# Kernel tuning notes

Measured on AMD Instinct MI355X. Metric: run time of the kernel, lower is better.

Reference implementation:

```python
import jax, jax.numpy as jnp
import numpy as np

V, E, H, L = 32000, 256, 512, 2
B, S, T = 32, 128, 128

def _run_lstm(xs, layers, h0, c0):
    # xs: [B,T,in]; layers: list of (Wih[4H,in], Whh[4H,H], bih[4H], bhh[4H]); h0,c0: [L,B,H]
    def step(carry, x):
        h, c = carry
        inp = x
        hs, cs = [], []
        for l, (Wih, Whh, bih, bhh) in enumerate(layers):
            g = inp @ Wih.T + h[l] @ Whh.T + bih + bhh
            i, f, gg, o = jnp.split(g, 4, axis=-1)  # torch gate order: i, f, g, o
            cn = jax.nn.sigmoid(f) * c[l] + jax.nn.sigmoid(i) * jnp.tanh(gg)
            hn = jax.nn.sigmoid(o) * jnp.tanh(cn)
            hs.append(hn); cs.append(cn); inp = hn
        return (jnp.stack(hs), jnp.stack(cs)), inp
    (hT, cT), ys = jax.lax.scan(step, (h0, c0), jnp.swapaxes(xs, 0, 1))
    return jnp.swapaxes(ys, 0, 1), hT, cT

def setup_inputs():
    key = jax.random.key(0)
    ks = jax.random.split(key, 24)
    k = 1.0 / np.sqrt(H)
    u = lambda kk, shape: jax.random.uniform(kk, shape, jnp.float32, -k, k)
    inp = {
        "src": jax.random.randint(ks[0], (B, S), 0, V),
        "tgt": jax.random.randint(ks[1], (B, T), 0, V),
        "emb": jax.random.normal(ks[2], (V, E), jnp.float32) * 0.02,
        "Wout": u(ks[3], (V, H)),
        "bout": u(ks[4], (V,)),
    }
    i = 5
    for pre in ("enc", "dec"):
        for l in range(L):
            din = E if l == 0 else H
            inp[pre + "_Wih" + str(l)] = u(ks[i], (4 * H, din)); i += 1
            inp[pre + "_Whh" + str(l)] = u(ks[i], (4 * H, H)); i += 1
            inp[pre + "_bih" + str(l)] = u(ks[i], (4 * H,)); i += 1
            inp[pre + "_bhh" + str(l)] = u(ks[i], (4 * H,)); i += 1
    return inp

def reference(src, tgt, emb, Wout, bout,
              enc_Wih0, enc_Whh0, enc_bih0, enc_bhh0,
              enc_Wih1, enc_Whh1, enc_bih1, enc_bhh1,
              dec_Wih0, dec_Whh0, dec_bih0, dec_bhh0,
              dec_Wih1, dec_Whh1, dec_bih1, dec_bhh1):
    enc_layers = [(enc_Wih0, enc_Whh0, enc_bih0, enc_bhh0),
                  (enc_Wih1, enc_Whh1, enc_bih1, enc_bhh1)]
    dec_layers = [(dec_Wih0, dec_Whh0, dec_bih0, dec_bhh0),
                  (dec_Wih1, dec_Whh1, dec_bih1, dec_bhh1)]
    h0 = jnp.zeros((L, src.shape[0], H), jnp.float32)
    c0 = jnp.zeros_like(h0)
    src_embed = emb[src]                                   # [B,S,E]; dropout = identity (eval)
    _, hT, cT = _run_lstm(src_embed, enc_layers, h0, c0)
    tgt_embed = emb[tgt]                                   # full teacher forcing (ratio=1.0)
    dec_out, _, _ = _run_lstm(tgt_embed, dec_layers, hT, cT)  # [B,T,H]
    logits = jnp.einsum('bth,vh->btv', dec_out, Wout) + bout  # [B,T,V]
    return logits
```

## Files before the change

### kernel.cpp

```cpp
#include <hip/hip_runtime.h>
#include <math.h>

#define Bsz 32
#define Hd  512
#define SEQ 128
#define G4H 2048
#define BH  16384
#define BARSTRIDE 32
#define SLOT 16384

typedef __attribute__((ext_vector_type(8))) short bf16x8;
typedef __attribute__((ext_vector_type(4))) float f32x4;
typedef __attribute__((ext_vector_type(4))) unsigned short us4;

__device__ __forceinline__ void gload16(const void* g, void* l) {
  __builtin_amdgcn_global_load_lds(
      (const __attribute__((address_space(1))) unsigned int*)g,
      (__attribute__((address_space(3))) unsigned int*)l, 16, 0, 0);
}

__global__ __launch_bounds__(256) void bias_sum_k(const float* __restrict__ a,
                                                  const float* __restrict__ b,
                                                  float* __restrict__ out) {
  int i = blockIdx.x * 256 + threadIdx.x;
  if (i < G4H) out[i] = a[i] + b[i];
}

__global__ __launch_bounds__(256) void embed_k(const int* __restrict__ idx,
                                               const float* __restrict__ emb,
                                               float* __restrict__ out) {
  int t = blockIdx.x * 256 + threadIdx.x;
  int m = t >> 6, e4 = (t & 63) << 2;
  *(float4*)&out[(size_t)m * 256 + e4] =
      *(const float4*)&emb[(size_t)idx[m] * 256 + e4];
}

__global__ __launch_bounds__(256) void split_k(const float* __restrict__ X,
                                               unsigned short* __restrict__ hi,
                                               unsigned short* __restrict__ lo) {
  int i = (blockIdx.x * 256 + threadIdx.x) << 2;
  float4 x = *(const float4*)&X[i];
  const float* xp = (const float*)&x;
  us4 h, l;
  #pragma unroll
  for (int e = 0; e < 4; ++e) {
    float v = xp[e];
    unsigned int u = __float_as_uint(v);
    unsigned int hr = (u + 0x7fffu + ((u >> 16) & 1u)) & 0xffff0000u;
    h[e] = (unsigned short)(hr >> 16);
    float rem = v - __uint_as_float(hr);
    unsigned int u2 = __float_as_uint(rem);
    l[e] = (unsigned short)((u2 + 0x7fffu + ((u2 >> 16) & 1u)) >> 16);
  }
  *(us4*)&hi[i] = h;
  *(us4*)&lo[i] = l;
}

__global__ __launch_bounds__(256) void pack_wbf_k(const float* __restrict__ W,
                                                  unsigned short* __restrict__ out) {
  __shared__ float Wl[16][512];
// ... 66 lines not shown
    for (int mf = 0; mf < 4; ++mf) {
      afh[mf] = *(const bf16x8*)&Ash[(wr * 64 + mf * 16 + fr) * 32 + fk];
      afl[mf] = *(const bf16x8*)&Asl[(wr * 64 + mf * 16 + fr) * 32 + fk];
    }
    #pragma unroll
    for (int nf = 0; nf < 4; ++nf) {
      bfh[nf] = *(const bf16x8*)&Bsh[(wc * 64 + nf * 16 + fr) * 32 + fk];
      bfl[nf] = *(const bf16x8*)&Bsl[(wc * 64 + nf * 16 + fr) * 32 + fk];
    }
    #pragma unroll
    for (int mf = 0; mf < 4; ++mf)
      #pragma unroll
      for (int nf = 0; nf < 4; ++nf) {
        acc[mf][nf] = __builtin_amdgcn_mfma_f32_16x16x32_bf16(afh[mf], bfh[nf],
                                                              acc[mf][nf], 0, 0, 0);
        acc[mf][nf] = __builtin_amdgcn_mfma_f32_16x16x32_bf16(afh[mf], bfl[nf],
                                                              acc[mf][nf], 0, 0, 0);
        acc[mf][nf] = __builtin_amdgcn_mfma_f32_16x16x32_bf16(afl[mf], bfh[nf],
                                                              acc[mf][nf], 0, 0, 0);
      }
    __syncthreads();
  }

  const int rgrp = (lane >> 4) << 2;
  #pragma unroll
  for (int nf = 0; nf < 4; ++nf) {
    int n = n0 + wc * 64 + nf * 16 + fr;
    float bn = bias[n];
    #pragma unroll
    for (int mf = 0; mf < 4; ++mf) {
      #pragma unroll
      for (int r = 0; r < 4; ++r) {
        int m = m0 + wr * 64 + mf * 16 + rgrp + r;
        C[(size_t)m * ldc + n] = acc[mf][nf][r] + bn;
      }
    }
  }
}

__device__ __forceinline__ void pollwait(const int* arr, int target) {
  const int tid = threadIdx.x;
  if (tid < 64) {
    const int* p0 = &arr[tid * BARSTRIDE];
    const int* p1 = &arr[(tid + 64) * BARSTRIDE];
    for (;;) {
      int a = __hip_atomic_load(p0, __ATOMIC_RELAXED, __HIP_MEMORY_SCOPE_AGENT);
      int b = __hip_atomic_load(p1, __ATOMIC_RELAXED, __HIP_MEMORY_SCOPE_AGENT);
      if (__all(min(a, b) >= target)) break;
      __builtin_amdgcn_s_sleep(1);
    }
  }
  __syncthreads();
}

__global__ __launch_bounds__(256, 1)
void lstm_seq_k(const unsigned short* __restrict__ pw0,
                const unsigned short* __restrict__ pw1a,
                const unsigned short* __restrict__ pw1b,
                const float* __restrict__ x0pre,
                const float* __restrict__ bias1,
                unsigned short* __restrict__ h0hi, unsigned short* __restrict__ h0lo,
                unsigned short* __restrict__ h1hi, unsigned short* __restrict__ h1lo,
                const unsigned short* __restrict__ h0ihi, const unsigned short* __restrict__ h0ilo,
                const unsigned short* __restrict__ h1ihi, const unsigned short* __restrict__ h1ilo,
                const float* __restrict__ c0init, const float* __restrict__ c1init,
                float* __restrict__ c0fin, float* __restrict__ c1fin,
                int* __restrict__ flag)
{
  __shared__ unsigned short wlds[49152];
  __shared__ float gpart[6528];
  __shared__ float gx[512];
  __shared__ unsigned short hstage[512];

  const int blk = blockIdx.x, tid = threadIdx.x;
  const int w = tid >> 6, lane = tid & 63;
  const int fr = lane & 15, fgk = (lane >> 4) << 3;

  {
    const uint4* s0 = (const uint4*)(pw0 + (size_t)blk * 16384);
    const uint4* s1 = (const uint4*)(pw1a + (size_t)blk * 16384);
    const uint4* s2 = (const uint4*)(pw1b + (size_t)blk * 16384);
    uint4* d = (uint4*)wlds;
    for (int i = tid; i < 2048; i += 256) {
      d[i] = s0[i]; d[2048 + i] = s1[i]; d[4096 + i] = s2[i];
    }
  }

  const int cl = (tid >> 5) & 3, b2 = tid & 31;
  const int nn = blk * 4 + cl;
  float creg, bv0 = 0.f, bv1 = 0.f, bv2 = 0.f, bv3 = 0.f;
  if (tid < 128) {
    creg = c0init[b2 * 512 + nn];
  } else {
    creg = c1init[b2 * 512 + nn];
    bv0 = bias1[nn]; bv1 = bias1[512 + nn];
    bv2 = bias1[1024 + nn]; bv3 = bias1[1536 + nn];
  }
  const int xcol = tid & 15, xb = tid >> 4;
  const int xj = (xcol >> 2) * 512 + blk * 4 + (xcol & 3);
  __syncthreads();

  #pragma unroll 1
  for (int u = 0; u <= SEQ; ++u) {
    const bool doL0 = (u < SEQ), doL1 = (u >= 1);

    float xv0 = 0.f, xv1 = 0.f;
    if (doL0) {
      xv0 = x0pre[((size_t)xb * SEQ + u) * G4H + xj];
      xv1 = x0pre[((size_t)(xb + 16) * SEQ + u) * G4H + xj];
    }

    if (u > 0) pollwait(flag, u);

    if (doL0) { gx[xcol * 32 + xb] = xv0; gx[xcol * 32 + xb + 16] = xv1; }

    const unsigned short* hAh = (u == 0) ? h0ihi : h0hi + (size_t)(u - 1) * SLOT;
    const unsigned short* hAl = (u == 0) ? h0ilo : h0lo + (size_t)(u - 1) * SLOT;
    const unsigned short* hBh = (u <= 1) ? h1ihi : h1hi + (size_t)(u - 2) * SLOT;
    const unsigned short* hBl = (u <= 1) ? h1ilo : h1lo + (size_t)(u - 2) * SLOT;

    f32x4 acc[3][2];
    #pragma unroll
    for (int m = 0; m < 3; ++m) {
      acc[m][0] = (f32x4){0.f, 0.f, 0.f, 0.f};
      acc[m][1] = (f32x4){0.f, 0.f, 0.f, 0.f};
    }

    #pragma unroll
    for (int q = 0; q < 4; ++q) {
      const int kf = (w << 2) + q;
      const int ko = (kf << 5) + fgk;
      const int wko = (kf << 9) + lane * 8;
      bf16x8 ah0 = *(const bf16x8*)&hAh[(size_t)fr * 512 + ko];
      bf16x8 al0 = *(const bf16x8*)&hAl[(size_t)fr * 512 + ko];
      bf16x8 ah1 = *(const bf16x8*)&hAh[(size_t)(fr + 16) * 512 + ko];
      bf16x8 al1 = *(const bf16x8*)&hAl[(size_t)(fr + 16) * 512 + ko];
      if (doL0) {
        bf16x8 bh = *(const bf16x8*)&wlds[wko];
        bf16x8 bl = *(const bf16x8*)&wlds[8192 + wko];
        acc[0][0] = __builtin_amdgcn_mfma_f32_16x16x32_bf16(ah0, bh, acc[0][0], 0, 0, 0);
        acc[0][0] = __builtin_amdgcn_mfma_f32_16x16x32_bf16(ah0, bl, acc[0][0], 0, 0, 0);
        acc[0][0] = __builtin_amdgcn_mfma_f32_16x16x32_bf16(al0, bh, acc[0][0], 0, 0, 0);
        acc[0][1] = __builtin_amdgcn_mfma_f32_16x16x32_bf16(ah1, bh, acc[0][1], 0, 0, 0);
        acc[0][1] = __builtin_amdgcn_mfma_f32_16x16x32_bf16(ah1, bl, acc[0][1], 0, 0, 0);
        acc[0][1] = __builtin_amdgcn_mfma_f32_16x16x32_bf16(al1, bh, acc[0][1], 0, 0, 0);
      }
      if (doL1) {
        bf16x8 bh = *(const bf16x8*)&wlds[16384 + wko];
        bf16x8 bl = *(const bf16x8*)&wlds[16384 + 8192 + wko];
        acc[1][0] = __builtin_amdgcn_mfma_f32_16x16x32_bf16(ah0, bh, acc[1][0], 0, 0, 0);
        acc[1][0] = __builtin_amdgcn_mfma_f32_16x16x32_bf16(ah0, bl, acc[1][0], 0, 0, 0);
        acc[1][0] = __builtin_amdgcn_mfma_f32_16x16x32_bf16(al0, bh, acc[1][0], 0, 0, 0);
        acc[1][1] = __builtin_amdgcn_mfma_f32_16x16x32_bf16(ah1, bh, acc[1][1], 0, 0, 0);
        acc[1][1] = __builtin_amdgcn_mfma_f32_16x16x32_bf16(ah1, bl, acc[1][1], 0, 0, 0);
        acc[1][1] = __builtin_amdgcn_mfma_f32_16x16x32_bf16(al1, bh, acc[1][1], 0, 0, 0);
        bf16x8 ch0 = *(const bf16x8*)&hBh[(size_t)fr * 512 + ko];
        bf16x8 cl0 = *(const bf16x8*)&hBl[(size_t)fr * 512 + ko];
        bf16x8 ch1 = *(const bf16x8*)&hBh[(size_t)(fr + 16) * 512 + ko];
        bf16x8 cl1 = *(const bf16x8*)&hBl[(size_t)(fr + 16) * 512 + ko];
        bf16x8 dh = *(const bf16x8*)&wlds[32768 + wko];
        bf16x8 dl = *(const bf16x8*)&wlds[32768 + 8192 + wko];
        acc[2][0] = __builtin_amdgcn_mfma_f32_16x16x32_bf16(ch0, dh, acc[2][0], 0, 0, 0);
        acc[2][0] = __builtin_amdgcn_mfma_f32_16x16x32_bf16(ch0, dl, acc[2][0], 0, 0, 0);
        acc[2][0] = __builtin_amdgcn_mfma_f32_16x16x32_bf16(cl0, dh, acc[2][0], 0, 0, 0);
        acc[2][1] = __builtin_amdgcn_mfma_f32_16x16x32_bf16(ch1, dh, acc[2][1], 0, 0, 0);
        acc[2][1] = __builtin_amdgcn_mfma_f32_16x16x32_bf16(ch1, dl, acc[2][1], 0, 0, 0);
        acc[2][1] = __builtin_amdgcn_mfma_f32_16x16x32_bf16(cl1, dh, acc[2][1], 0, 0, 0);
      }
    }

    #pragma unroll
    for (int m = 0; m < 3; ++m)
      #pragma unroll
      for (int mf = 0; mf < 2; ++mf)
        #pragma unroll
        for (int j = 0; j < 4; ++j)
          gpart[(m * 4 + w) * 544 + (mf * 16 + (lane >> 4) * 4 + j) * 17 + fr] = acc[m][mf][j];
    __syncthreads();

    if (tid < 128) {
      if (doL0) {
        float g[4];
        #pragma unroll
        for (int gt = 0; gt < 4; ++gt) {
          float s = gx[(gt * 4 + cl) * 32 + b2];
          #pragma unroll
          for (int ww = 0; ww < 4; ++ww)
            s += gpart[ww * 544 + b2 * 17 + gt * 4 + cl];
          g[gt] = s;
        }
        float i_ = 1.f / (1.f + expf(-g[0]));
        float f_ = 1.f / (1.f + expf(-g[1]));
        float gg = tanhf(g[2]);
        float o_ = 1.f / (1.f + expf(-g[3]));
        float cn = f_ * creg + i_ * gg;
        float hn = o_ * tanhf(cn);
        creg = cn;
        unsigned int uu = __float_as_uint(hn);
        unsigned int hr = (uu + 0x7fffu + ((uu >> 16) & 1u)) & 0xffff0000u;
        float rem = hn - __uint_as_float(hr);
        unsigned int u2 = __float_as_uint(rem);
        hstage[(0 * 32 + b2) * 4 + cl] = (unsigned short)(hr >> 16);
        hstage[(1 * 32 + b2) * 4 + cl] =
            (unsigned short)((u2 + 0x7fffu + ((u2 >> 16) & 1u)) >> 16);
      }
    } else {
      if (doL1) {
        float g[4];
        #pragma unroll
        for (int gt = 0; gt < 4; ++gt) {
          float s = 0.f;
          #pragma unroll
          for (int ww = 0; ww < 4; ++ww)
            s += gpart[(4 + ww) * 544 + b2 * 17 + gt * 4 + cl]
               + gpart[(8 + ww) * 544 + b2 * 17 + gt * 4 + cl];
          g[gt] = s;
        }
        g[0] += bv0; g[1] += bv1; g[2] += bv2; g[3] += bv3;
        float i_ = 1.f / (1.f + expf(-g[0]));
        float f_ = 1.f / (1.f + expf(-g[1]));
        float gg = tanhf(g[2]);
        float o_ = 1.f / (1.f + expf(-g[3]));
        float cn = f_ * creg + i_ * gg;
        float hn = o_ * tanhf(cn);
        creg = cn;
        unsigned int uu = __float_as_uint(hn);
        unsigned int hr = (uu + 0x7fffu + ((uu >> 16) & 1u)) & 0xffff0000u;
        float rem = hn - __uint_as_float(hr);
        unsigned int u2 = __float_as_uint(rem);
        hstage[(2 * 32 + b2) * 4 + cl] = (unsigned short)(hr >> 16);
        hstage[(3 * 32 + b2) * 4 + cl] =
            (unsigned short)((u2 + 0x7fffu + ((u2 >> 16) & 1u)) >> 16);
      }
    }
    __syncthreads();

    if (tid < 128) {
      int layer = tid >> 6, hl = (tid >> 5) & 1, bb = tid & 31;
      bool go = layer ? doL1 : doL0;
      if (go) {
        unsigned long long v =
            *(const unsigned long long*)&hstage[((layer * 2 + hl) * 32 + bb) * 4];
        unsigned short* arr = layer ? (hl ? h1lo : h1hi) : (hl ? h0lo : h0hi);
        int slot = layer ? (u - 1) : u;
        __hip_atomic_store((unsigned long long*)&arr[(size_t)slot * SLOT + bb * 512 + blk * 4],
                           v, __ATOMIC_RELAXED, __HIP_MEMORY_SCOPE_AGENT);
      }
    }
    asm volatile("s_waitcnt vmcnt(0)" ::: "memory");
    __syncthreads();
    if (tid == 0)
      __hip_atomic_store(&flag[blk * BARSTRIDE], u + 1,
                         __ATOMIC_RELAXED, __HIP_MEMORY_SCOPE_AGENT);
  }

  if (tid < 128) c0fin[b2 * 512 + nn] = creg;
  else           c1fin[b2 * 512 + nn] = creg;
}

extern "C" void kernel_launch(void* const* d_in, const int* in_sizes, int n_in,
                              void* d_out, int out_size, void* d_ws, size_t ws_size,
                              hipStream_t stream) {
  const int*   src  = (const int*)d_in[0];
  const int*   tgt  = (const int*)d_in[1];
  const float* emb  = (const float*)d_in[2];
  const float* Wout = (const float*)d_in[3];
  const float* bout = (const float*)d_in[4];
  const float* eWih0 = (const float*)d_in[5];
  const float* eWhh0 = (const float*)d_in[6];
  const float* ebih0 = (const float*)d_in[7];
  const float* ebhh0 = (const float*)d_in[8];
  const float* eWih1 = (const float*)d_in[9];
  const float* eWhh1 = (const float*)d_in[10];
  const float* ebih1 = (const float*)d_in[11];
  const float* ebhh1 = (const float*)d_in[12];
  const float* dWih0 = (const float*)d_in[13];
  const float* dWhh0 = (const float*)d_in[14];
  const float* dbih0 = (const float*)d_in[15];
  const float* dbhh0 = (const float*)d_in[16];
  const float* dWih1 = (const float*)d_in[17];
  const float* dWhh1 = (const float*)d_in[18];
  const float* dbih1 = (const float*)d_in[19];
  const float* dbhh1 = (const float*)d_in[20];

  if (ws_size < 86245376ull) return;

  float* ws = (float*)d_ws;
  char*  wsb = (char*)d_ws;
  unsigned short* PK   = (unsigned short*)(wsb + 37748736);
  unsigned short* PW0E = PK;
  unsigned short* PW1AE = PK + 2097152;
  unsigned short* PW1BE = PK + 4194304;
  unsigned short* PW0D = PK + 6291456;
  unsigned short* PW1AD = PK + 8388608;
  unsigned short* PW1BD = PK + 10485760;
  const size_t OFF_EMB  = 0;
  const size_t OFF_X0   = 1048576;
  const size_t OFF_BS0E = 15728640;
  const size_t OFF_B1E  = 15730688;
  const size_t OFF_BS0D = 15732736;
  const size_t OFF_B1D  = 15734784;
  const size_t OFF_Z    = 15736832;
  const size_t OFF_BAR  = 15753216;
  const size_t OFF_C0   = 15761408;
  const size_t OFF_C1   = 15777792;
  unsigned short* Ehi  = (unsigned short*)(wsb + 63176704);
  unsigned short* Elo  = (unsigned short*)(wsb + 65273856);
  unsigned short* WIhi = (unsigned short*)(wsb + 67371008);
  unsigned short* WIlo = (unsigned short*)(wsb + 68419584);
  unsigned short* H0hi = (unsigned short*)(wsb + 69468160);
  unsigned short* H0lo = (unsigned short*)(wsb + 73662464);
  unsigned short* H1hi = (unsigned short*)(wsb + 77856768);
  unsigned short* H1lo = (unsigned short*)(wsb + 82051072);
  unsigned short* Bhi  = (unsigned short*)(wsb + 0);
  unsigned short* Blo  = (unsigned short*)(wsb + 32768000);
  const unsigned short* ZU = (const unsigned short*)(ws + OFF_Z);
  const float* ZF = ws + OFF_Z;

  int* eflag = (int*)(ws + OFF_BAR);
  int* dflag = eflag + 4096;

  pack_wbf_k<<<128, 256, 0, stream>>>(eWhh0, PW0E);
  pack_wbf_k<<<128, 256, 0, stream>>>(eWih1, PW1AE);
  pack_wbf_k<<<128, 256, 0, stream>>>(eWhh1, PW1BE);
  pack_wbf_k<<<128, 256, 0, stream>>>(dWhh0, PW0D);
  pack_wbf_k<<<128, 256, 0, stream>>>(dWih1, PW1AD);
  pack_wbf_k<<<128, 256, 0, stream>>>(dWhh1, PW1BD);
  bias_sum_k<<<8, 256, 0, stream>>>(ebih0, ebhh0, ws + OFF_BS0E);
  bias_sum_k<<<8, 256, 0, stream>>>(ebih1, ebhh1, ws + OFF_B1E);
  bias_sum_k<<<8, 256, 0, stream>>>(dbih0, dbhh0, ws + OFF_BS0D);
  bias_sum_k<<<8, 256, 0, stream>>>(dbih1, dbhh1, ws + OFF_B1D);

  hipMemsetAsync(ws + OFF_Z, 0, 98304, stream);

  embed_k<<<1024, 256, 0, stream>>>(src, emb, ws + OFF_EMB);
  split_k<<<1024, 256, 0, stream>>>(ws + OFF_EMB, Ehi, Elo);
  split_k<<<512, 256, 0, stream>>>(eWih0, WIhi, WIlo);
  gemm_bfs_k<<<dim3(32, 16), 256, 0, stream>>>(Ehi, Elo, WIhi, WIlo,
                                               ws + OFF_BS0E, ws + OFF_X0, 256, 2048, 0);
  lstm_seq_k<<<128, 256, 0, stream>>>(PW0E, PW1AE, PW1BE,
                                      ws + OFF_X0, ws + OFF_B1E,
                                      H0hi, H0lo, H1hi, H1lo,
                                      ZU, ZU, ZU, ZU,
                                      ZF, ZF,
                                      ws + OFF_C0, ws + OFF_C1,
                                      eflag);

  embed_k<<<1024, 256, 0, stream>>>(tgt, emb, ws + OFF_EMB);
  split_k<<<1024, 256, 0, stream>>>(ws + OFF_EMB, Ehi, Elo);
  split_k<<<512, 256, 0, stream>>>(dWih0, WIhi, WIlo);
  gemm_bfs_k<<<dim3(32, 16), 256, 0, stream>>>(Ehi, Elo, WIhi, WIlo,
                                               ws + OFF_BS0D, ws + OFF_X0, 256, 2048, 0);
  lstm_seq_k<<<128, 256, 0, stream>>>(PW0D, PW1AD, PW1BD,
                                      ws + OFF_X0, ws + OFF_B1D,
                                      H0hi, H0lo, H1hi, H1lo,
                                      H0hi + (size_t)127 * SLOT, H0lo + (size_t)127 * SLOT,
                                      H1hi + (size_t)127 * SLOT, H1lo + (size_t)127 * SLOT,
                                      ws + OFF_C0, ws + OFF_C1,
                                      ws + OFF_C0, ws + OFF_C1,
                                      dflag);

  split_k<<<16000, 256, 0, stream>>>(Wout, Bhi, Blo);
  gemm_bfs_k<<<dim3(32, 250), 256, 0, stream>>>(H1hi, H1lo, Bhi, Blo,
                                                bout, (float*)d_out, 512, 32000, 1);
}
```

Before: 2.220 ms.

## Split LSTM layer phases with separate flags to overlap layer-1 and layer-0 steps

Restructures the persistent two-layer LSTM loop so each iteration first does layer 1 for step u-2, publishes a layer-1 flag, then does layer 0 for step u with its own flag barrier. Layer 0 no longer waits for layer-1 completion in the same barrier. This shortens the critical path of the layer-0 recurrence, which now only depends on the previous layer-0 step. In exchange it adds a second grid-wide poll per iteration, an extra loop iteration, and relocated flag and cell-state buffers in the workspace.

```diff
diff --git a/kernel.cpp b/kernel.cpp
--- a/kernel.cpp
+++ b/kernel.cpp
@@ -178,6 +178,21 @@
   }
   __syncthreads();
 }
+__device__ __forceinline__ void pollwait2(const int* a1, int t1,
+                                          const int* a0, int t0) {
+  const int tid = threadIdx.x;
+  if (tid < 64) {
+    for (;;) {
+      int a = __hip_atomic_load(&a1[tid * BARSTRIDE], __ATOMIC_RELAXED, __HIP_MEMORY_SCOPE_AGENT);
+      int b = __hip_atomic_load(&a1[(tid + 64) * BARSTRIDE], __ATOMIC_RELAXED, __HIP_MEMORY_SCOPE_AGENT);
+      int c = __hip_atomic_load(&a0[tid * BARSTRIDE], __ATOMIC_RELAXED, __HIP_MEMORY_SCOPE_AGENT);
+      int d = __hip_atomic_load(&a0[(tid + 64) * BARSTRIDE], __ATOMIC_RELAXED, __HIP_MEMORY_SCOPE_AGENT);
+      if (__all(min(a, b) >= t1 && min(c, d) >= t0)) break;
+      __builtin_amdgcn_s_sleep(1);
+    }
+  }
+  __syncthreads();
+}
 
 __global__ __launch_bounds__(256, 1)
 void lstm_seq_k(const unsigned short* __restrict__ pw0,
@@ -191,7 +206,7 @@
                 const unsigned short* __restrict__ h1ihi, const unsigned short* __restrict__ h1ilo,
                 const float* __restrict__ c0init, const float* __restrict__ c1init,
                 float* __restrict__ c0fin, float* __restrict__ c1fin,
-                int* __restrict__ flag)
+                int* __restrict__ flag0, int* __restrict__ flag1)
 {
   __shared__ unsigned short wlds[49152];
   __shared__ float gpart[6528];
@@ -227,8 +242,9 @@
   __syncthreads();
 
   #pragma unroll 1
-  for (int u = 0; u <= SEQ; ++u) {
-    const bool doL0 = (u < SEQ), doL1 = (u >= 1);
+  for (int u = 0; u <= SEQ + 1; ++u) {
+    const bool doL0 = (u < SEQ), doL1 = (u >= 2);
+    const int t1 = u - 2;
 
     float xv0 = 0.f, xv1 = 0.f;
     if (doL0) {
@@ -236,102 +252,61 @@
       xv1 = x0pre[((size_t)(xb + 16) * SEQ + u) * G4H + xj];
     }
 
-    if (u > 0) pollwait(flag, u);
-
-    if (doL0) { gx[xcol * 32 + xb] = xv0; gx[xcol * 32 + xb + 16] = xv1; }
-
-    const unsigned short* hAh = (u == 0) ? h0ihi : h0hi + (size_t)(u - 1) * SLOT;
-    const unsigned short* hAl = (u == 0) ? h0ilo : h0lo + (size_t)(u - 1) * SLOT;
-    const unsigned short* hBh = (u <= 1) ? h1ihi : h1hi + (size_t)(u - 2) * SLOT;
-    const unsigned short* hBl = (u <= 1) ? h1ilo : h1lo + (size_t)(u - 2) * SLOT;
-
-    f32x4 acc[3][2];
-    #pragma unroll
-    for (int m = 0; m < 3; ++m) {
-      acc[m][0] = (f32x4){0.f, 0.f, 0.f, 0.f};
-      acc[m][1] = (f32x4){0.f, 0.f, 0.f, 0.f};
-    }
-
-    #pragma unroll
-    for (int q = 0; q < 4; ++q) {
-      const int kf = (w << 2) + q;
-      const int ko = (kf << 5) + fgk;
-      const int wko = (kf << 9) + lane * 8;
-      bf16x8 ah0 = *(const bf16x8*)&hAh[(size_t)fr * 512 + ko];
-      bf16x8 al0 = *(const bf16x8*)&hAl[(size_t)fr * 512 + ko];
-      bf16x8 ah1 = *(const bf16x8*)&hAh[(size_t)(fr + 16) * 512 + ko];
-      bf16x8 al1 = *(const bf16x8*)&hAl[(size_t)(fr + 16) * 512 + ko];
-      if (doL0) {
-        bf16x8 bh = *(const bf16x8*)&wlds[wko];
-        bf16x8 bl = *(const bf16x8*)&wlds[8192 + wko];
+    if (u >= 1) pollwait2(flag1, u - 1, flag0, u - 1);
+
+    if (doL1) {
+      const unsigned short* hAh = h0hi + (size_t)t1 * SLOT;
+      const unsigned short* hAl = h0lo + (size_t)t1 * SLOT;
+      const unsigned short* hBh = (t1 == 0) ? h1ihi : h1hi + (size_t)(t1 - 1) * SLOT;
+      const unsigned short* hBl = (t1 == 0) ? h1ilo : h1lo + (size_t)(t1 - 1) * SLOT;
+
+      f32x4 acc[2][2];
+      #pragma unroll
+      for (int m = 0; m < 2; ++m) {
+        acc[m][0] = (f32x4){0.f, 0.f, 0.f, 0.f};
+        acc[m][1] = (f32x4){0.f, 0.f, 0.f, 0.f};
+      }
+      #pragma unroll
+      for (int q = 0; q < 4; ++q) {
+        const int kf = (w << 2) + q;
+        const int ko = (kf << 5) + fgk;
+        const int wko = (kf << 9) + lane * 8;
+        bf16x8 ah0 = *(const bf16x8*)&hAh[(size_t)fr * 512 + ko];
+        bf16x8 al0 = *(const bf16x8*)&hAl[(size_t)fr * 512 + ko];
+        bf16x8 ah1 = *(const bf16x8*)&hAh[(size_t)(fr + 16) * 512 + ko];
+        bf16x8 al1 = *(const bf16x8*)&hAl[(size_t)(fr + 16) * 512 + ko];
+        bf16x8 bh = *(const bf16x8*)&wlds[16384 + wko];
+        bf16x8 bl = *(const bf16x8*)&wlds[16384 + 8192 + wko];
         acc[0][0] = __builtin_amdgcn_mfma_f32_16x16x32_bf16(ah0, bh, acc[0][0], 0, 0, 0);
         acc[0][0] = __builtin_amdgcn_mfma_f32_16x16x32_bf16(ah0, bl, acc[0][0], 0, 0, 0);
         acc[0][0] = __builtin_amdgcn_mfma_f32_16x16x32_bf16(al0, bh, acc[0][0], 0, 0, 0);
         acc[0][1] = __builtin_amdgcn_mfma_f32_16x16x32_bf16(ah1, bh, acc[0][1], 0, 0, 0);
         acc[0][1] = __builtin_amdgcn_mfma_f32_16x16x32_bf16(ah1, bl, acc[0][1], 0, 0, 0);
         acc[0][1] = __builtin_amdgcn_mfma_f32_16x16x32_bf16(al1, bh, acc[0][1], 0, 0, 0);
-      }
-      if (doL1) {
-        bf16x8 bh = *(const bf16x8*)&wlds[16384 + wko];
-        bf16x8 bl = *(const bf16x8*)&wlds[16384 + 8192 + wko];
-        acc[1][0] = __builtin_amdgcn_mfma_f32_16x16x32_bf16(ah0, bh, acc[1][0], 0, 0, 0);
-        acc[1][0] = __builtin_amdgcn_mfma_f32_16x16x32_bf16(ah0, bl, acc[1][0], 0, 0, 0);
-        acc[1][0] = __builtin_amdgcn_mfma_f32_16x16x32_bf16(al0, bh, acc[1][0], 0, 0, 0);
-        acc[1][1] = __builtin_amdgcn_mfma_f32_16x16x32_bf16(ah1, bh, acc[1][1], 0, 0, 0);
-        acc[1][1] = __builtin_amdgcn_mfma_f32_16x16x32_bf16(ah1, bl, acc[1][1], 0, 0, 0);
-        acc[1][1] = __builtin_amdgcn_mfma_f32_16x16x32_bf16(al1, bh, acc[1][1], 0, 0, 0);
         bf16x8 ch0 = *(const bf16x8*)&hBh[(size_t)fr * 512 + ko];
         bf16x8 cl0 = *(const bf16x8*)&hBl[(size_t)fr * 512 + ko];
         bf16x8 ch1 = *(const bf16x8*)&hBh[(size_t)(fr + 16) * 512 + ko];
         bf16x8 cl1 = *(const bf16x8*)&hBl[(size_t)(fr + 16) * 512 + ko];
         bf16x8 dh = *(const bf16x8*)&wlds[32768 + wko];
         bf16x8 dl = *(const bf16x8*)&wlds[32768 + 8192 + wko];
-        acc[2][0] = __builtin_amdgcn_mfma_f32_16x16x32_bf16(ch0, dh, acc[2][0], 0, 0, 0);
-        acc[2][0] = __builtin_amdgcn_mfma_f32_16x16x32_bf16(ch0, dl, acc[2][0], 0, 0, 0);
-        acc[2][0] = __builtin_amdgcn_mfma_f32_16x16x32_bf16(cl0, dh, acc[2][0], 0, 0, 0);
-        acc[2][1] = __builtin_amdgcn_mfma_f32_16x16x32_bf16(ch1, dh, acc[2][1], 0, 0, 0);
-        acc[2][1] = __builtin_amdgcn_mfma_f32_16x16x32_bf16(ch1, dl, acc[2][1], 0, 0, 0);
-        acc[2][1] = __builtin_amdgcn_mfma_f32_16x16x32_bf16(cl1, dh, acc[2][1], 0, 0, 0);
-      }
-    }
-
-    #pragma unroll
-    for (int m = 0; m < 3; ++m)
-      #pragma unroll
-      for (int mf = 0; mf < 2; ++mf)
+        acc[1][0] = __builtin_amdgcn_mfma_f32_16x16x32_bf16(ch0, dh, acc[1][0], 0, 0, 0);
+        acc[1][0] = __builtin_amdgcn_mfma_f32_16x16x32_bf16(ch0, dl, acc[1][0], 0, 0, 0);
+        acc[1][0] = __builtin_amdgcn_mfma_f32_16x16x32_bf16(cl0, dh, acc[1][0], 0, 0, 0);
+        acc[1][1] = __builtin_amdgcn_mfma_f32_16x16x32_bf16(ch1, dh, acc[1][1], 0, 0, 0);
+        acc[1][1] = __builtin_amdgcn_mfma_f32_16x16x32_bf16(ch1, dl, acc[1][1], 0, 0, 0);
+        acc[1][1] = __builtin_amdgcn_mfma_f32_16x16x32_bf16(cl1, dh, acc[1][1], 0, 0, 0);
+      }
+      #pragma unroll
+      for (int m = 0; m < 2; ++m)
         #pragma unroll
-        for (int j = 0; j < 4; ++j)
-          gpart[(m * 4 + w) * 544 + (mf * 16 + (lane >> 4) * 4 + j) * 17 + fr] = acc[m][mf][j];
-    __syncthreads();
-
-    if (tid < 128) {
-      if (doL0) {
-        float g[4];
-        #pragma unroll
-        for (int gt = 0; gt < 4; ++gt) {
-          float s = gx[(gt * 4 + cl) * 32 + b2];
+        for (int mf = 0; mf < 2; ++mf)
           #pragma unroll
-          for (int ww = 0; ww < 4; ++ww)
-            s += gpart[ww * 544 + b2 * 17 + gt * 4 + cl];
-          g[gt] = s;
-        }
-        float i_ = 1.f / (1.f + expf(-g[0]));
-        float f_ = 1.f / (1.f + expf(-g[1]));
-        float gg = tanhf(g[2]);
-        float o_ = 1.f / (1.f + expf(-g[3]));
-        float cn = f_ * creg + i_ * gg;
-        float hn = o_ * tanhf(cn);
-        creg = cn;
-        unsigned int uu = __float_as_uint(hn);
-        unsigned int hr = (uu + 0x7fffu + ((uu >> 16) & 1u)) & 0xffff0000u;
-        float rem = hn - __uint_as_float(hr);
-        unsigned int u2 = __float_as_uint(rem);
-        hstage[(0 * 32 + b2) * 4 + cl] = (unsigned short)(hr >> 16);
-        hstage[(1 * 32 + b2) * 4 + cl] =
-            (unsigned short)((u2 + 0x7fffu + ((u2 >> 16) & 1u)) >> 16);
-      }
-    } else {
-      if (doL1) {
+          for (int j = 0; j < 4; ++j)
+            gpart[((m + 1) * 4 + w) * 544 + (mf * 16 + (lane >> 4) * 4 + j) * 17 + fr]
+                = acc[m][mf][j];
+      __syncthreads();
+
+      if (tid >= 128) {
         float g[4];
         #pragma unroll
         for (int gt = 0; gt < 4; ++gt) {
@@ -358,26 +333,100 @@
         hstage[(3 * 32 + b2) * 4 + cl] =
             (unsigned short)((u2 + 0x7fffu + ((u2 >> 16) & 1u)) >> 16);
       }
-    }
-    __syncthreads();
-
-    if (tid < 128) {
-      int layer = tid >> 6, hl = (tid >> 5) & 1, bb = tid & 31;
-      bool go = layer ? doL1 : doL0;
-      if (go) {
+      __syncthreads();
+
+      if (tid >= 64 && tid < 128) {
+        int hl = (tid >> 5) & 1, bb = tid & 31;
         unsigned long long v =
-            *(const unsigned long long*)&hstage[((layer * 2 + hl) * 32 + bb) * 4];
-        unsigned short* arr = layer ? (hl ? h1lo : h1hi) : (hl ? h0lo : h0hi);
-        int slot = layer ? (u - 1) : u;
-        __hip_atomic_store((unsigned long long*)&arr[(size_t)slot * SLOT + bb * 512 + blk * 4],
+            *(const unsigned long long*)&hstage[((2 + hl) * 32 + bb) * 4];
+        unsigned short* arr = hl ? h1lo : h1hi;
+        __hip_atomic_store((unsigned long long*)&arr[(size_t)t1 * SLOT + bb * 512 + blk * 4],
                            v, __ATOMIC_RELAXED, __HIP_MEMORY_SCOPE_AGENT);
       }
-    }
-    asm volatile("s_waitcnt vmcnt(0)" ::: "memory");
-    __syncthreads();
+      asm volatile("s_waitcnt vmcnt(0)" ::: "memory");
+      __syncthreads();
+    }
     if (tid == 0)
-      __hip_atomic_store(&flag[blk * BARSTRIDE], u + 1,
+      __hip_atomic_store(&flag1[blk * BARSTRIDE], u,
                          __ATOMIC_RELAXED, __HIP_MEMORY_SCOPE_AGENT);
+
+    if (doL0) {
+      pollwait(flag0, u);
+
+      gx[xcol * 32 + xb] = xv0; gx[xcol * 32 + xb + 16] = xv1;
+
+      const unsigned short* hAh = (u == 0) ? h0ihi : h0hi + (size_t)(u - 1) * SLOT;
+      const unsigned short* hAl = (u == 0) ? h0ilo : h0lo + (size_t)(u - 1) * SLOT;
+
+      f32x4 acc0[2];
+      acc0[0] = (f32x4){0.f, 0.f, 0.f, 0.f};
+      acc0[1] = (f32x4){0.f, 0.f, 0.f, 0.f};
+      #pragma unroll
+      for (int q = 0; q < 4; ++q) {
+        const int kf = (w << 2) + q;
+        const int ko = (kf << 5) + fgk;
+        const int wko = (kf << 9) + lane * 8;
+        bf16x8 ah0 = *(const bf16x8*)&hAh[(size_t)fr * 512 + ko];
+        bf16x8 al0 = *(const bf16x8*)&hAl[(size_t)fr * 512 + ko];
+        bf16x8 ah1 = *(const bf16x8*)&hAh[(size_t)(fr + 16) * 512 + ko];
+        bf16x8 al1 = *(const bf16x8*)&hAl[(size_t)(fr + 16) * 512 + ko];
+        bf16x8 bh = *(const bf16x8*)&wlds[wko];
+        bf16x8 bl = *(const bf16x8*)&wlds[8192 + wko];
+        acc0[0] = __builtin_amdgcn_mfma_f32_16x16x32_bf16(ah0, bh, acc0[0], 0, 0, 0);
+        acc0[0] = __builtin_amdgcn_mfma_f32_16x16x32_bf16(ah0, bl, acc0[0], 0, 0, 0);
+        acc0[0] = __builtin_amdgcn_mfma_f32_16x16x32_bf16(al0, bh, acc0[0], 0, 0, 0);
+        acc0[1] = __builtin_amdgcn_mfma_f32_16x16x32_bf16(ah1, bh, acc0[1], 0, 0, 0);
+        acc0[1] = __builtin_amdgcn_mfma_f32_16x16x32_bf16(ah1, bl, acc0[1], 0, 0, 0);
+        acc0[1] = __builtin_amdgcn_mfma_f32_16x16x32_bf16(al1, bh, acc0[1], 0, 0, 0);
+      }
+      #pragma unroll
+      for (int mf = 0; mf < 2; ++mf)
+        #pragma unroll
+        for (int j = 0; j < 4; ++j)
+          gpart[w * 544 + (mf * 16 + (lane >> 4) * 4 + j) * 17 + fr] = acc0[mf][j];
+      __syncthreads();
+
+      if (tid < 128) {
+        float g[4];
+        #pragma unroll
+        for (int gt = 0; gt < 4; ++gt) {
+          float s = gx[(gt * 4 + cl) * 32 + b2];
+          #pragma unroll
+          for (int ww = 0; ww < 4; ++ww)
+            s += gpart[ww * 544 + b2 * 17 + gt * 4 + cl];
+          g[gt] = s;
+        }
+        float i_ = 1.f / (1.f + expf(-g[0]));
+        float f_ = 1.f / (1.f + expf(-g[1]));
+        float gg = tanhf(g[2]);
+        float o_ = 1.f / (1.f + expf(-g[3]));
+        float cn = f_ * creg + i_ * gg;
+        float hn = o_ * tanhf(cn);
+        creg = cn;
+        unsigned int uu = __float_as_uint(hn);
+        unsigned int hr = (uu + 0x7fffu + ((uu >> 16) & 1u)) & 0xffff0000u;
+        float rem = hn - __uint_as_float(hr);
+        unsigned int u2 = __float_as_uint(rem);
+        hstage[(0 * 32 + b2) * 4 + cl] = (unsigned short)(hr >> 16);
+        hstage[(1 * 32 + b2) * 4 + cl] =
+            (unsigned short)((u2 + 0x7fffu + ((u2 >> 16) & 1u)) >> 16);
+      }
+      __syncthreads();
+
+      if (tid < 64) {
+        int hl = (tid >> 5) & 1, bb = tid & 31;
+        unsigned long long v =
+            *(const unsigned long long*)&hstage[(hl * 32 + bb) * 4];
+        unsigned short* arr = hl ? h0lo : h0hi;
+        __hip_atomic_store((unsigned long long*)&arr[(size_t)u * SLOT + bb * 512 + blk * 4],
+                           v, __ATOMIC_RELAXED, __HIP_MEMORY_SCOPE_AGENT);
+      }
+      asm volatile("s_waitcnt vmcnt(0)" ::: "memory");
+      __syncthreads();
+      if (tid == 0)
+        __hip_atomic_store(&flag0[blk * BARSTRIDE], u + 1,
+                           __ATOMIC_RELAXED, __HIP_MEMORY_SCOPE_AGENT);
+    }
   }
 
   if (tid < 128) c0fin[b2 * 512 + nn] = creg;
@@ -409,7 +458,7 @@
   const float* dbih1 = (const float*)d_in[19];
   const float* dbhh1 = (const float*)d_in[20];
 
-  if (ws_size < 86245376ull) return;
+  if (ws_size < 86376448ull) return;
 
   float* ws = (float*)d_ws;
   char*  wsb = (char*)d_ws;
@@ -427,9 +476,6 @@
   const size_t OFF_BS0D = 15732736;
   const size_t OFF_B1D  = 15734784;
   const size_t OFF_Z    = 15736832;
-  const size_t OFF_BAR  = 15753216;
-  const size_t OFF_C0   = 15761408;
-  const size_t OFF_C1   = 15777792;
   unsigned short* Ehi  = (unsigned short*)(wsb + 63176704);
   unsigned short* Elo  = (unsigned short*)(wsb + 65273856);
   unsigned short* WIhi = (unsigned short*)(wsb + 67371008);
@@ -440,11 +486,13 @@
   unsigned short* H1lo = (unsigned short*)(wsb + 82051072);
   unsigned short* Bhi  = (unsigned short*)(wsb + 0);
   unsigned short* Blo  = (unsigned short*)(wsb + 32768000);
+  float* C0f = (float*)(wsb + 86245376);
+  float* C1f = (float*)(wsb + 86310912);
   const unsigned short* ZU = (const unsigned short*)(ws + OFF_Z);
   const float* ZF = ws + OFF_Z;
 
-  int* eflag = (int*)(ws + OFF_BAR);
-  int* dflag = eflag + 4096;
+  int* fb = (int*)(wsb + 63012864);
+  int* e0 = fb, *e1 = fb + 4096, *d0 = fb + 8192, *d1 = fb + 12288;
 
   pack_wbf_k<<<128, 256, 0, stream>>>(eWhh0, PW0E);
   pack_wbf_k<<<128, 256, 0, stream>>>(eWih1, PW1AE);
@@ -457,7 +505,7 @@
   bias_sum_k<<<8, 256, 0, stream>>>(dbih0, dbhh0, ws + OFF_BS0D);
   bias_sum_k<<<8, 256, 0, stream>>>(dbih1, dbhh1, ws + OFF_B1D);
 
-  hipMemsetAsync(ws + OFF_Z, 0, 98304, stream);
+  hipMemsetAsync(ws + OFF_Z, 0, 131072, stream);
 
   embed_k<<<1024, 256, 0, stream>>>(src, emb, ws + OFF_EMB);
   split_k<<<1024, 256, 0, stream>>>(ws + OFF_EMB, Ehi, Elo);
@@ -469,8 +517,8 @@
                                       H0hi, H0lo, H1hi, H1lo,
                                       ZU, ZU, ZU, ZU,
                                       ZF, ZF,
-                                      ws + OFF_C0, ws + OFF_C1,
-                                      eflag);
+                                      C0f, C1f,
+                                      e0, e1);
 
   embed_k<<<1024, 256, 0, stream>>>(tgt, emb, ws + OFF_EMB);
   split_k<<<1024, 256, 0, stream>>>(ws + OFF_EMB, Ehi, Elo);
@@ -482,9 +530,9 @@
                                       H0hi, H0lo, H1hi, H1lo,
                                       H0hi + (size_t)127 * SLOT, H0lo + (size_t)127 * SLOT,
                                       H1hi + (size_t)127 * SLOT, H1lo + (size_t)127 * SLOT,
-                                      ws + OFF_C0, ws + OFF_C1,
-                                      ws + OFF_C0, ws + OFF_C1,
-                                      dflag);
+                                      C0f, C1f,
+                                      C0f, C1f,
+                                      d0, d1);
 
   split_k<<<16000, 256, 0, stream>>>(Wout, Bhi, Blo);
   gemm_bfs_k<<<dim3(32, 250), 256, 0, stream>>>(H1hi, H1lo, Bhi, Blo,
```

After: 2.859 ms. 1.29x slower.

## Split LSTM recurrence batch into two independent 16-row domains over 256 blocks

Applied to the files above, without the earlier changes.

The persistent LSTM kernel now launches 256 blocks instead of 128. Each pair of blocks shares the same hidden-column slice but owns half of the batch, and each half-batch domain has its own flag barrier. This halves the MFMA work, h loads and gate math per block per timestep, and spreads the recurrence over more CUs so the per-step critical path is shorter. The cost is that weights are staged into LDS twice, more blocks touch the flag arrays, and the flags and cell-state buffers move to a new workspace layout with a larger zeroed region.

```diff
diff --git a/kernel.cpp b/kernel.cpp
--- a/kernel.cpp
+++ b/kernel.cpp
@@ -5,7 +5,6 @@
 #define Hd  512
 #define SEQ 128
 #define G4H 2048
-#define BH  16384
 #define BARSTRIDE 32
 #define SLOT 16384
 
@@ -191,197 +190,179 @@
                 const unsigned short* __restrict__ h1ihi, const unsigned short* __restrict__ h1ilo,
                 const float* __restrict__ c0init, const float* __restrict__ c1init,
                 float* __restrict__ c0fin, float* __restrict__ c1fin,
-                int* __restrict__ flag)
+                int* __restrict__ flagbase)
 {
   __shared__ unsigned short wlds[49152];
-  __shared__ float gpart[6528];
-  __shared__ float gx[512];
-  __shared__ unsigned short hstage[512];
+  __shared__ float gpart[3264];
+  __shared__ float gx[256];
+  __shared__ unsigned short hstage[256];
 
   const int blk = blockIdx.x, tid = threadIdx.x;
+  const int dom = blk & 1, cb = blk >> 1;
+  const int bb0 = dom << 4;
+  int* flag = flagbase + dom * 4096;
   const int w = tid >> 6, lane = tid & 63;
   const int fr = lane & 15, fgk = (lane >> 4) << 3;
 
   {
-    const uint4* s0 = (const uint4*)(pw0 + (size_t)blk * 16384);
-    const uint4* s1 = (const uint4*)(pw1a + (size_t)blk * 16384);
-    const uint4* s2 = (const uint4*)(pw1b + (size_t)blk * 16384);
+    const uint4* s0 = (const uint4*)(pw0 + (size_t)cb * 16384);
+    const uint4* s1 = (const uint4*)(pw1a + (size_t)cb * 16384);
+    const uint4* s2 = (const uint4*)(pw1b + (size_t)cb * 16384);
     uint4* d = (uint4*)wlds;
     for (int i = tid; i < 2048; i += 256) {
       d[i] = s0[i]; d[2048 + i] = s1[i]; d[4096 + i] = s2[i];
     }
   }
 
-  const int cl = (tid >> 5) & 3, b2 = tid & 31;
-  const int nn = blk * 4 + cl;
-  float creg, bv0 = 0.f, bv1 = 0.f, bv2 = 0.f, bv3 = 0.f;
-  if (tid < 128) {
-    creg = c0init[b2 * 512 + nn];
-  } else {
-    creg = c1init[b2 * 512 + nn];
+  const int b2 = tid & 15, cl = (tid >> 4) & 3;
+  const int nn = cb * 4 + cl;
+  const int gb = bb0 + b2;
+  float creg = 0.f, bv0 = 0.f, bv1 = 0.f, bv2 = 0.f, bv3 = 0.f;
+  if (tid < 64) {
+    creg = c0init[gb * 512 + nn];
+  } else if (tid < 128) {
+    creg = c1init[gb * 512 + nn];
     bv0 = bias1[nn]; bv1 = bias1[512 + nn];
     bv2 = bias1[1024 + nn]; bv3 = bias1[1536 + nn];
   }
-  const int xcol = tid & 15, xb = tid >> 4;
-  const int xj = (xcol >> 2) * 512 + blk * 4 + (xcol & 3);
+  const int xcol = tid & 15, xb = (tid >> 4) & 15;
+  const int xj = (xcol >> 2) * 512 + cb * 4 + (xcol & 3);
+  const int xgb = bb0 + xb;
   __syncthreads();
 
   #pragma unroll 1
   for (int u = 0; u <= SEQ; ++u) {
     const bool doL0 = (u < SEQ), doL1 = (u >= 1);
 
-    float xv0 = 0.f, xv1 = 0.f;
-    if (doL0) {
-      xv0 = x0pre[((size_t)xb * SEQ + u) * G4H + xj];
-      xv1 = x0pre[((size_t)(xb + 16) * SEQ + u) * G4H + xj];
-    }
+    float xv = doL0 ? x0pre[((size_t)xgb * SEQ + u) * G4H + xj] : 0.f;
 
     if (u > 0) pollwait(flag, u);
 
-    if (doL0) { gx[xcol * 32 + xb] = xv0; gx[xcol * 32 + xb + 16] = xv1; }
+    if (doL0) gx[xcol * 16 + xb] = xv;
 
     const unsigned short* hAh = (u == 0) ? h0ihi : h0hi + (size_t)(u - 1) * SLOT;
     const unsigned short* hAl = (u == 0) ? h0ilo : h0lo + (size_t)(u - 1) * SLOT;
     const unsigned short* hBh = (u <= 1) ? h1ihi : h1hi + (size_t)(u - 2) * SLOT;
     const unsigned short* hBl = (u <= 1) ? h1ilo : h1lo + (size_t)(u - 2) * SLOT;
 
-    f32x4 acc[3][2];
-    #pragma unroll
-    for (int m = 0; m < 3; ++m) {
-      acc[m][0] = (f32x4){0.f, 0.f, 0.f, 0.f};
-      acc[m][1] = (f32x4){0.f, 0.f, 0.f, 0.f};
-    }
+    f32x4 acc[3];
+    acc[0] = (f32x4){0.f, 0.f, 0.f, 0.f};
+    acc[1] = (f32x4){0.f, 0.f, 0.f, 0.f};
+    acc[2] = (f32x4){0.f, 0.f, 0.f, 0.f};
 
     #pragma unroll
     for (int q = 0; q < 4; ++q) {
       const int kf = (w << 2) + q;
       const int ko = (kf << 5) + fgk;
       const int wko = (kf << 9) + lane * 8;
-      bf16x8 ah0 = *(const bf16x8*)&hAh[(size_t)fr * 512 + ko];
-      bf16x8 al0 = *(const bf16x8*)&hAl[(size_t)fr * 512 + ko];
-      bf16x8 ah1 = *(const bf16x8*)&hAh[(size_t)(fr + 16) * 512 + ko];
-      bf16x8 al1 = *(const bf16x8*)&hAl[(size_t)(fr + 16) * 512 + ko];
+      const size_t arow = (size_t)(bb0 + fr) * 512 + ko;
+      bf16x8 ah = *(const bf16x8*)&hAh[arow];
+      bf16x8 al = *(const bf16x8*)&hAl[arow];
       if (doL0) {
         bf16x8 bh = *(const bf16x8*)&wlds[wko];
         bf16x8 bl = *(const bf16x8*)&wlds[8192 + wko];
-        acc[0][0] = __builtin_amdgcn_mfma_f32_16x16x32_bf16(ah0, bh, acc[0][0], 0, 0, 0);
-        acc[0][0] = __builtin_amdgcn_mfma_f32_16x16x32_bf16(ah0, bl, acc[0][0], 0, 0, 0);
-        acc[0][0] = __builtin_amdgcn_mfma_f32_16x16x32_bf16(al0, bh, acc[0][0], 0, 0, 0);
-        acc[0][1] = __builtin_amdgcn_mfma_f32_16x16x32_bf16(ah1, bh, acc[0][1], 0, 0, 0);
-        acc[0][1] = __builtin_amdgcn_mfma_f32_16x16x32_bf16(ah1, bl, acc[0][1], 0, 0, 0);
-        acc[0][1] = __builtin_amdgcn_mfma_f32_16x16x32_bf16(al1, bh, acc[0][1], 0, 0, 0);
+        acc[0] = __builtin_amdgcn_mfma_f32_16x16x32_bf16(ah, bh, acc[0], 0, 0, 0);
+        acc[0] = __builtin_amdgcn_mfma_f32_16x16x32_bf16(ah, bl, acc[0], 0, 0, 0);
+        acc[0] = __builtin_amdgcn_mfma_f32_16x16x32_bf16(al, bh, acc[0], 0, 0, 0);
       }
       if (doL1) {
         bf16x8 bh = *(const bf16x8*)&wlds[16384 + wko];
         bf16x8 bl = *(const bf16x8*)&wlds[16384 + 8192 + wko];
-        acc[1][0] = __builtin_amdgcn_mfma_f32_16x16x32_bf16(ah0, bh, acc[1][0], 0, 0, 0);
-        acc[1][0] = __builtin_amdgcn_mfma_f32_16x16x32_bf16(ah0, bl, acc[1][0], 0, 0, 0);
-        acc[1][0] = __builtin_amdgcn_mfma_f32_16x16x32_bf16(al0, bh, acc[1][0], 0, 0, 0);
-        acc[1][1] = __builtin_amdgcn_mfma_f32_16x16x32_bf16(ah1, bh, acc[1][1], 0, 0, 0);
-        acc[1][1] = __builtin_amdgcn_mfma_f32_16x16x32_bf16(ah1, bl, acc[1][1], 0, 0, 0);
-        acc[1][1] = __builtin_amdgcn_mfma_f32_16x16x32_bf16(al1, bh, acc[1][1], 0, 0, 0);
-        bf16x8 ch0 = *(const bf16x8*)&hBh[(size_t)fr * 512 + ko];
-        bf16x8 cl0 = *(const bf16x8*)&hBl[(size_t)fr * 512 + ko];
-        bf16x8 ch1 = *(const bf16x8*)&hBh[(size_t)(fr + 16) * 512 + ko];
-        bf16x8 cl1 = *(const bf16x8*)&hBl[(size_t)(fr + 16) * 512 + ko];
+        acc[1] = __builtin_amdgcn_mfma_f32_16x16x32_bf16(ah, bh, acc[1], 0, 0, 0);
+        acc[1] = __builtin_amdgcn_mfma_f32_16x16x32_bf16(ah, bl, acc[1], 0, 0, 0);
+        acc[1] = __builtin_amdgcn_mfma_f32_16x16x32_bf16(al, bh, acc[1], 0, 0, 0);
+        bf16x8 ch = *(const bf16x8*)&hBh[arow];
+        bf16x8 cl8 = *(const bf16x8*)&hBl[arow];
         bf16x8 dh = *(const bf16x8*)&wlds[32768 + wko];
         bf16x8 dl = *(const bf16x8*)&wlds[32768 + 8192 + wko];
-        acc[2][0] = __builtin_amdgcn_mfma_f32_16x16x32_bf16(ch0, dh, acc[2][0], 0, 0, 0);
-        acc[2][0] = __builtin_amdgcn_mfma_f32_16x16x32_bf16(ch0, dl, acc[2][0], 0, 0, 0);
-        acc[2][0] = __builtin_amdgcn_mfma_f32_16x16x32_bf16(cl0, dh, acc[2][0], 0, 0, 0);
-        acc[2][1] = __builtin_amdgcn_mfma_f32_16x16x32_bf16(ch1, dh, acc[2][1], 0, 0, 0);
-        acc[2][1] = __builtin_amdgcn_mfma_f32_16x16x32_bf16(ch1, dl, acc[2][1], 0, 0, 0);
-        acc[2][1] = __builtin_amdgcn_mfma_f32_16x16x32_bf16(cl1, dh, acc[2][1], 0, 0, 0);
+        acc[2] = __builtin_amdgcn_mfma_f32_16x16x32_bf16(ch, dh, acc[2], 0, 0, 0);
+        acc[2] = __builtin_amdgcn_mfma_f32_16x16x32_bf16(ch, dl, acc[2], 0, 0, 0);
+        acc[2] = __builtin_amdgcn_mfma_f32_16x16x32_bf16(cl8, dh, acc[2], 0, 0, 0);
       }
     }
 
     #pragma unroll
     for (int m = 0; m < 3; ++m)
       #pragma unroll
-      for (int mf = 0; mf < 2; ++mf)
+      for (int j = 0; j < 4; ++j)
+        gpart[(m * 4 + w) * 272 + ((lane >> 4) * 4 + j) * 17 + fr] = acc[m][j];
+    __syncthreads();
+
+    if (tid < 64 && doL0) {
+      float g[4];
+      #pragma unroll
+      for (int gt = 0; gt < 4; ++gt) {
+        float s = gx[(gt * 4 + cl) * 16 + b2];
         #pragma unroll
-        for (int j = 0; j < 4; ++j)
-          gpart[(m * 4 + w) * 544 + (mf * 16 + (lane >> 4) * 4 + j) * 17 + fr] = acc[m][mf][j];
+        for (int ww = 0; ww < 4; ++ww)
+          s += gpart[ww * 272 + b2 * 17 + gt * 4 + cl];
+        g[gt] = s;
+      }
+      float i_ = 1.f / (1.f + expf(-g[0]));
+      float f_ = 1.f / (1.f + expf(-g[1]));
+      float gg = tanhf(g[2]);
+      float o_ = 1.f / (1.f + expf(-g[3]));
+      float cn = f_ * creg + i_ * gg;
+      float hn = o_ * tanhf(cn);
+      creg = cn;
+      unsigned int uu = __float_as_uint(hn);
+      unsigned int hr = (uu + 0x7fffu + ((uu >> 16) & 1u)) & 0xffff0000u;
+      float rem = hn - __uint_as_float(hr);
+      unsigned int u2 = __float_as_uint(rem);
+      hstage[(0 * 16 + b2) * 4 + cl] = (unsigned short)(hr >> 16);
+      hstage[(1 * 16 + b2) * 4 + cl] =
+          (unsigned short)((u2 + 0x7fffu + ((u2 >> 16) & 1u)) >> 16);
+    } else if (tid >= 64 && tid < 128 && doL1) {
+      float g[4];
+      #pragma unroll
+      for (int gt = 0; gt < 4; ++gt) {
+        float s = 0.f;
+        #pragma unroll
+        for (int ww = 0; ww < 4; ++ww)
+          s += gpart[(4 + ww) * 272 + b2 * 17 + gt * 4 + cl]
+             + gpart[(8 + ww) * 272 + b2 * 17 + gt * 4 + cl];
+        g[gt] = s;
+      }
+      g[0] += bv0; g[1] += bv1; g[2] += bv2; g[3] += bv3;
+      float i_ = 1.f / (1.f + expf(-g[0]));
+      float f_ = 1.f / (1.f + expf(-g[1]));
+      float gg = tanhf(g[2]);
+      float o_ = 1.f / (1.f + expf(-g[3]));
+      float cn = f_ * creg + i_ * gg;
+      float hn = o_ * tanhf(cn);
+      creg = cn;
+      unsigned int uu = __float_as_uint(hn);
+      unsigned int hr = (uu + 0x7fffu + ((uu >> 16) & 1u)) & 0xffff0000u;
+      float rem = hn - __uint_as_float(hr);
+      unsigned int u2 = __float_as_uint(rem);
+      hstage[(2 * 16 + b2) * 4 + cl] = (unsigned short)(hr >> 16);
+      hstage[(3 * 16 + b2) * 4 + cl] =
+          (unsigned short)((u2 + 0x7fffu + ((u2 >> 16) & 1u)) >> 16);
+    }
     __syncthreads();
 
-    if (tid < 128) {
-      if (doL0) {
-        float g[4];
-        #pragma unroll
-        for (int gt = 0; gt < 4; ++gt) {
-          float s = gx[(gt * 4 + cl) * 32 + b2];
-          #pragma unroll
-          for (int ww = 0; ww < 4; ++ww)
-            s += gpart[ww * 544 + b2 * 17 + gt * 4 + cl];
-          g[gt] = s;
-        }
-        float i_ = 1.f / (1.f + expf(-g[0]));
-        float f_ = 1.f / (1.f + expf(-g[1]));
-        float gg = tanhf(g[2]);
-        float o_ = 1.f / (1.f + expf(-g[3]));
-        float cn = f_ * creg + i_ * gg;
-        float hn = o_ * tanhf(cn);
-        creg = cn;
-        unsigned int uu = __float_as_uint(hn);
-        unsigned int hr = (uu + 0x7fffu + ((uu >> 16) & 1u)) & 0xffff0000u;
-        float rem = hn - __uint_as_float(hr);
-        unsigned int u2 = __float_as_uint(rem);
-        hstage[(0 * 32 + b2) * 4 + cl] = (unsigned short)(hr >> 16);
-        hstage[(1 * 32 + b2) * 4 + cl] =
-            (unsigned short)((u2 + 0x7fffu + ((u2 >> 16) & 1u)) >> 16);
-      }
-    } else {
-      if (doL1) {
-        float g[4];
-        #pragma unroll
-        for (int gt = 0; gt < 4; ++gt) {
-          float s = 0.f;
-          #pragma unroll
-          for (int ww = 0; ww < 4; ++ww)
-            s += gpart[(4 + ww) * 544 + b2 * 17 + gt * 4 + cl]
-               + gpart[(8 + ww) * 544 + b2 * 17 + gt * 4 + cl];
-          g[gt] = s;
-        }
-        g[0] += bv0; g[1] += bv1; g[2] += bv2; g[3] += bv3;
-        float i_ = 1.f / (1.f + expf(-g[0]));
-        float f_ = 1.f / (1.f + expf(-g[1]));
-        float gg = tanhf(g[2]);
-        float o_ = 1.f / (1.f + expf(-g[3]));
-        float cn = f_ * creg + i_ * gg;
-        float hn = o_ * tanhf(cn);
-        creg = cn;
-        unsigned int uu = __float_as_uint(hn);
-        unsigned int hr = (uu + 0x7fffu + ((uu >> 16) & 1u)) & 0xffff0000u;
-        float rem = hn - __uint_as_float(hr);
-        unsigned int u2 = __float_as_uint(rem);
-        hstage[(2 * 32 + b2) * 4 + cl] = (unsigned short)(hr >> 16);
-        hstage[(3 * 32 + b2) * 4 + cl] =
-            (unsigned short)((u2 + 0x7fffu + ((u2 >> 16) & 1u)) >> 16);
-      }
-    }
-    __syncthreads();
-
-    if (tid < 128) {
-      int layer = tid >> 6, hl = (tid >> 5) & 1, bb = tid & 31;
+    if (tid < 64) {
+      int layer = (tid >> 5) & 1, hl = (tid >> 4) & 1, bb = tid & 15;
       bool go = layer ? doL1 : doL0;
       if (go) {
         unsigned long long v =
-            *(const unsigned long long*)&hstage[((layer * 2 + hl) * 32 + bb) * 4];
+            *(const unsigned long long*)&hstage[((layer * 2 + hl) * 16 + bb) * 4];
         unsigned short* arr = layer ? (hl ? h1lo : h1hi) : (hl ? h0lo : h0hi);
         int slot = layer ? (u - 1) : u;
-        __hip_atomic_store((unsigned long long*)&arr[(size_t)slot * SLOT + bb * 512 + blk * 4],
-                           v, __ATOMIC_RELAXED, __HIP_MEMORY_SCOPE_AGENT);
+        __hip_atomic_store(
+            (unsigned long long*)&arr[(size_t)slot * SLOT + (bb0 + bb) * 512 + cb * 4],
+            v, __ATOMIC_RELAXED, __HIP_MEMORY_SCOPE_AGENT);
       }
     }
     asm volatile("s_waitcnt vmcnt(0)" ::: "memory");
     __syncthreads();
     if (tid == 0)
-      __hip_atomic_store(&flag[blk * BARSTRIDE], u + 1,
+      __hip_atomic_store(&flag[cb * BARSTRIDE], u + 1,
                          __ATOMIC_RELAXED, __HIP_MEMORY_SCOPE_AGENT);
   }
 
-  if (tid < 128) c0fin[b2 * 512 + nn] = creg;
-  else           c1fin[b2 * 512 + nn] = creg;
+  if (tid < 64)        c0fin[gb * 512 + nn] = creg;
+  else if (tid < 128)  c1fin[gb * 512 + nn] = creg;
 }
 
 extern "C" void kernel_launch(void* const* d_in, const int* in_sizes, int n_in,
@@ -409,7 +390,7 @@
   const float* dbih1 = (const float*)d_in[19];
   const float* dbhh1 = (const float*)d_in[20];
 
-  if (ws_size < 86245376ull) return;
+  if (ws_size < 86376448ull) return;
 
   float* ws = (float*)d_ws;
   char*  wsb = (char*)d_ws;
@@ -427,9 +408,6 @@
   const size_t OFF_BS0D = 15732736;
   const size_t OFF_B1D  = 15734784;
   const size_t OFF_Z    = 15736832;
-  const size_t OFF_BAR  = 15753216;
-  const size_t OFF_C0   = 15761408;
-  const size_t OFF_C1   = 15777792;
   unsigned short* Ehi  = (unsigned short*)(wsb + 63176704);
   unsigned short* Elo  = (unsigned short*)(wsb + 65273856);
   unsigned short* WIhi = (unsigned short*)(wsb + 67371008);
@@ -440,11 +418,14 @@
   unsigned short* H1lo = (unsigned short*)(wsb + 82051072);
   unsigned short* Bhi  = (unsigned short*)(wsb + 0);
   unsigned short* Blo  = (unsigned short*)(wsb + 32768000);
+  float* C0f = (float*)(wsb + 86245376);
+  float* C1f = (float*)(wsb + 86310912);
   const unsigned short* ZU = (const unsigned short*)(ws + OFF_Z);
   const float* ZF = ws + OFF_Z;
 
-  int* eflag = (int*)(ws + OFF_BAR);
-  int* dflag = eflag + 4096;
+  int* fb = (int*)(wsb + 63012864);
+  int* eF = fb;
+  int* dF = fb + 8192;
 
   pack_wbf_k<<<128, 256, 0, stream>>>(eWhh0, PW0E);
   pack_wbf_k<<<128, 256, 0, stream>>>(eWih1, PW1AE);
@@ -457,34 +438,34 @@
   bias_sum_k<<<8, 256, 0, stream>>>(dbih0, dbhh0, ws + OFF_BS0D);
   bias_sum_k<<<8, 256, 0, stream>>>(dbih1, dbhh1, ws + OFF_B1D);
 
-  hipMemsetAsync(ws + OFF_Z, 0, 98304, stream);
+  hipMemsetAsync(ws + OFF_Z, 0, 131072, stream);
 
   embed_k<<<1024, 256, 0, stream>>>(src, emb, ws + OFF_EMB);
   split_k<<<1024, 256, 0, stream>>>(ws + OFF_EMB, Ehi, Elo);
   split_k<<<512, 256, 0, stream>>>(eWih0, WIhi, WIlo);
   gemm_bfs_k<<<dim3(32, 16), 256, 0, stream>>>(Ehi, Elo, WIhi, WIlo,
                                                ws + OFF_BS0E, ws + OFF_X0, 256, 2048, 0);
-  lstm_seq_k<<<128, 256, 0, stream>>>(PW0E, PW1AE, PW1BE,
+  lstm_seq_k<<<256, 256, 0, stream>>>(PW0E, PW1AE, PW1BE,
                                       ws + OFF_X0, ws + OFF_B1E,
                                       H0hi, H0lo, H1hi, H1lo,
                                       ZU, ZU, ZU, ZU,
                                       ZF, ZF,
-                                      ws + OFF_C0, ws + OFF_C1,
-                                      eflag);
+                                      C0f, C1f,
+                                      eF);
 
   embed_k<<<1024, 256, 0, stream>>>(tgt, emb, ws + OFF_EMB);
   split_k<<<1024, 256, 0, stream>>>(ws + OFF_EMB, Ehi, Elo);
   split_k<<<512, 256, 0, stream>>>(dWih0, WIhi, WIlo);
   gemm_bfs_k<<<dim3(32, 16), 256, 0, stream>>>(Ehi, Elo, WIhi, WIlo,
                                                ws + OFF_BS0D, ws + OFF_X0, 256, 2048, 0);
-  lstm_seq_k<<<128, 256, 0, stream>>>(PW0D, PW1AD, PW1BD,
+  lstm_seq_k<<<256, 256, 0, stream>>>(PW0D, PW1AD, PW1BD,
                                       ws + OFF_X0, ws + OFF_B1D,
                                       H0hi, H0lo, H1hi, H1lo,
                                       H0hi + (size_t)127 * SLOT, H0lo + (size_t)127 * SLOT,
                                       H1hi + (size_t)127 * SLOT, H1lo + (size_t)127 * SLOT,
-                                      ws + OFF_C0, ws + OFF_C1,
-                                      ws + OFF_C0, ws + OFF_C1,
-                                      dflag);
+                                      C0f, C1f,
+                                      C0f, C1f,
+                                      dF);
 
   split_k<<<16000, 256, 0, stream>>>(Wout, Bhi, Blo);
   gemm_bfs_k<<<dim3(32, 250), 256, 0, stream>>>(H1hi, H1lo, Bhi, Blo,
```

After: 1.913 ms. 13.8% less time.
